# Kernel optimization log

Measured on AMD Instinct MI355X. Metric: run time of the kernel, lower is better.

## Reference

```python
import jax, jax.numpy as jnp
import numpy as np

N_MIX = 2


def setup_inputs() -> dict:
    key = jax.random.key(0)
    k1, k2, k3, k4 = jax.random.split(key, 4)
    B, d_k, N = 8, 512, 2048
    qt = jax.random.normal(k1, (B, d_k, N), dtype=jnp.float32)
    kt = jax.random.normal(k2, (B, d_k, N), dtype=jnp.float32)
    vt = jax.random.normal(k3, (B, d_k, N), dtype=jnp.float32)
    std = N_MIX ** -0.5
    weight = jax.random.uniform(k4, (N_MIX, d_k), dtype=jnp.float32, minval=-std, maxval=std)
    return {"qt": qt, "kt": kt, "vt": vt, "weight": weight}


def reference(qt, kt, vt, weight):
    # qt: [B, d_k, N], kt: [B, d_k, N2], vt: [B, d_v, N2], weight: [m, d_k]
    B, d_k, N = qt.shape
    N2 = kt.shape[2]
    m = N_MIX
    d = d_k // m
    temperature = jnp.float32(d_k ** 0.5)  # note: sqrt(d_k), not sqrt(d)

    # mixture weights pi: softmax over the m mixture components
    bar_qt = jnp.mean(qt, axis=2)  # [B, d_k]
    pi = jax.nn.softmax(jnp.einsum('md,bd->bm', weight, bar_qt), axis=1)  # [B, m]
    pi = pi.reshape(B * m, 1, 1)

    q = jnp.transpose(qt.reshape(B * m, d, N), (0, 2, 1))  # [B*m, N, d]
    k = kt.reshape(B * m, d, N2)                            # [B*m, d, N2]
    v = jnp.transpose(vt, (0, 2, 1))                        # [B, N2, d_v]

    attn = jnp.matmul(q, k) / temperature                   # [B*m, N, N2]
    attn = jax.nn.softmax(attn, axis=2)
    # dropout is identity at inference
    attn = (attn * pi).reshape(B, m, N, N2).sum(axis=1)     # [B, N, N2]

    output = jnp.matmul(attn, v)                            # [B, N, d_v]
    return output, attn
```

## Files before the change

kernel.cpp:

```cpp
#include <hip/hip_runtime.h>
#include <stdint.h>

typedef unsigned short u16;
typedef float f32x4 __attribute__((ext_vector_type(4)));
typedef _Float16 half8 __attribute__((ext_vector_type(8)));
typedef __fp16 fp16x2 __attribute__((ext_vector_type(2)));

#define B_  8
#define M_  2
#define DK_ 512
#define D_  256
#define N_  2048
#define DV_ 512

#define OUT_FLOATS (B_*N_*DV_)
#define QB_U16     (B_*M_*N_*D_)

__device__ __forceinline__ uint32_t pk16(float a, float b){
    fp16x2 h = __builtin_amdgcn_cvt_pkrtz(a, b);
    return __builtin_bit_cast(uint32_t, h);
}
__device__ __forceinline__ float h2f_lo(uint32_t u){
    return (float)__builtin_bit_cast(_Float16, (unsigned short)(u & 0xffffu));
}
__device__ __forceinline__ float h2f_hi(uint32_t u){
    return (float)__builtin_bit_cast(_Float16, (unsigned short)(u >> 16));
}

__global__ __launch_bounds__(256) void k0_transpose(const float* __restrict__ qt,
                                                    const float* __restrict__ kt,
                                                    u16* __restrict__ dstBase,
                                                    float* __restrict__ wsBar){
    const int it = blockIdx.x, yc = blockIdx.y, z = blockIdx.z;
    const int b = z & 7, src = z >> 3;
    const float* sp = src ? kt : qt;
    u16* dp = dstBase + (size_t)src * QB_U16;
    const int m = yc >> 2;
    const int cbase = (yc & 3) * 64;
    const int i0 = it * 64;
    __shared__ u16 lds[64 * 72];
    const int t = threadIdx.x;
    {
        const int c_loc = t >> 2;
        const int iq = (t & 3) * 16;
        const float* g = sp + (size_t)(b*DK_ + m*D_ + cbase + c_loc) * N_ + i0 + iq;
        float vv[16];
        *(float4*)&vv[0]  = *(const float4*)(g + 0);
        *(float4*)&vv[4]  = *(const float4*)(g + 4);
        *(float4*)&vv[8]  = *(const float4*)(g + 8);
        *(float4*)&vv[12] = *(const float4*)(g + 12);
        #pragma unroll
        for (int e = 0; e < 16; ++e){
            _Float16 hf = (_Float16)vv[e];
            lds[(iq + e)*72 + c_loc] = __builtin_bit_cast(unsigned short, hf);
        }
        if (src == 0){
            float s = 0.f;
            #pragma unroll
            for (int e = 0; e < 16; ++e) s += vv[e];
            s += __shfl_xor(s, 1);
            s += __shfl_xor(s, 2);
            if ((t & 3) == 0)
                atomicAdd(&wsBar[b*DK_ + m*D_ + cbase + c_loc], s);
        }
    }
    __syncthreads();
    {
        const int i_loc = t >> 2;
        const int cq = (t & 3) * 16;
        uint4 a  = *(const uint4*)&lds[i_loc*72 + cq];
        uint4 b2 = *(const uint4*)&lds[i_loc*72 + cq + 8];
        u16* o = dp + (size_t)((b*M_ + m)*N_ + i0 + i_loc) * D_ + cbase + cq;
        *(uint4*)o = a;
        *(uint4*)(o + 8) = b2;
    }
}

__global__ __launch_bounds__(256) void k0_vconv(const float* __restrict__ vt,
                                                u16* __restrict__ vF){
    const int idx = blockIdx.x * 256 + threadIdx.x;
    const int dv = idx & 511;
    const int g  = (idx >> 9) & 3;
    const int jc = (idx >> 11) & 63;
    const int b  = idx >> 17;
    const float* src = vt + ((size_t)(b*DV_ + dv))*N_ + jc*32 + g*8;
    float4 f0 = *(const float4*)src;
    float4 f1 = *(const float4*)(src + 4);
    uint4 o;
    o.x = pk16(f0.x, f0.y);
    o.y = pk16(f0.z, f0.w);
    o.z = pk16(f1.x, f1.y);
    o.w = pk16(f1.z, f1.w);
    *(uint4*)(vF + (size_t)idx * 8) = o;
}

__global__ void k2_logits(const float* __restrict__ wgt,
                          const float* __restrict__ bar,
                          float* __restrict__ wsLog){
    const int bm = blockIdx.x;
    const int b = bm >> 1, m = bm & 1;
    const int l = threadIdx.x;
    float s = 0.f;
    #pragma unroll
    for (int k = 0; k < 8; ++k){
        const int c = l + k*64;
        s += wgt[m*DK_ + c] * bar[b*DK_ + c];
    }
    s += __shfl_xor(s, 1); s += __shfl_xor(s, 2); s += __shfl_xor(s, 4);
    s += __shfl_xor(s, 8); s += __shfl_xor(s, 16); s += __shfl_xor(s, 32);
    if (l == 0) wsLog[bm] = s * (1.f / (float)N_);
}

__global__ __launch_bounds__(256, 2) void k3_qk(const u16* __restrict__ qB,
                                                const u16* __restrict__ kB,
                                                uint32_t* __restrict__ attnE,
                                                float* __restrict__ wsSum){
    const int jt = blockIdx.x, it = blockIdx.y, b = blockIdx.z;
    const int t = threadIdx.x;
    const int w = t >> 6, l = t & 63;
    const int wi = w & 1, wj = w >> 1;
    const int l15 = l & 15, lq = l >> 4;
    __shared__ u16 lds[4 * 128 * 64];

    f32x4 acc[2][4][4] = {};

    const int srow = t >> 1, shalf = t & 1;
    for (int bk = 0; bk < 4; ++bk){
        #pragma unroll
        for (int tile = 0; tile < 4; ++tile){
            const int qk = tile >> 1, m = tile & 1;
            const u16* sp = qk ? kB : qB;
            const int row0 = (qk ? jt : it) * 128;
            const u16* g = sp + (size_t)((b*M_ + m)*N_ + row0 + srow) * D_ + bk*64 + shalf*32;
            const uint4* gp = (const uint4*)g;
            uint4 v0 = gp[0], v1 = gp[1], v2 = gp[2], v3 = gp[3];
            u16* base = &lds[(tile*128 + srow) * 64];
            const int rs = srow & 7;
            *(uint4*)&base[((shalf*4 + 0) ^ rs) * 8] = v0;
            *(uint4*)&base[((shalf*4 + 1) ^ rs) * 8] = v1;
            *(uint4*)&base[((shalf*4 + 2) ^ rs) * 8] = v2;
            *(uint4*)&base[((shalf*4 + 3) ^ rs) * 8] = v3;
        }
        __syncthreads();
        #pragma unroll
        for (int ks = 0; ks < 2; ++ks){
            #pragma unroll
            for (int m = 0; m < 2; ++m){
                half8 a[4], bb[4];
                #pragma unroll
                for (int ti = 0; ti < 4; ++ti){
                    const int row = wi*64 + ti*16 + l15;
                    const int gr = (ks*4 + lq) ^ (row & 7);
                    a[ti] = *(const half8*)&lds[(m*128 + row)*64 + gr*8];
                }
                #pragma unroll
                for (int tj = 0; tj < 4; ++tj){
                    const int row = wj*64 + tj*16 + l15;
                    const int gr = (ks*4 + lq) ^ (row & 7);
                    bb[tj] = *(const half8*)&lds[((2 + m)*128 + row)*64 + gr*8];
                }
                #pragma unroll
                for (int ti = 0; ti < 4; ++ti)
                    #pragma unroll
                    for (int tj = 0; tj < 4; ++tj)
                        acc[m][ti][tj] = __builtin_amdgcn_mfma_f32_16x16x32_f16(
                            a[ti], bb[tj], acc[m][ti][tj], 0, 0, 0);
            }
        }
        __syncthreads();
    }

    const float INVT = 0.04419417382415922f;
    uint32_t* op = attnE + (size_t)b * N_ * N_;
    const int ibase = it*128 + wi*64;
    const int jbase = jt*128 + wj*64;
    #pragma unroll
    for (int ti = 0; ti < 4; ++ti){
        float rs[2][4] = {};
        #pragma unroll
        for (int tj = 0; tj < 4; ++tj){
            #pragma unroll
            for (int rr = 0; rr < 4; ++rr){
                const int i = ibase + ti*16 + lq*4 + rr;
                const int j = jbase + tj*16 + l15;
                const float e0 = __expf(acc[0][ti][tj][rr] * INVT);
                const float e1 = __expf(acc[1][ti][tj][rr] * INVT);
                op[(size_t)i * N_ + j] = pk16(e0, e1);
                rs[0][rr] += e0;
                rs[1][rr] += e1;
            }
        }
        #pragma unroll
        for (int m2 = 0; m2 < 2; ++m2){
            #pragma unroll
            for (int rr = 0; rr < 4; ++rr){
                float s = rs[m2][rr];
                s += __shfl_xor(s, 1); s += __shfl_xor(s, 2);
                s += __shfl_xor(s, 4); s += __shfl_xor(s, 8);
                if (l15 == 0)
                    atomicAdd(&wsSum[(size_t)(b*M_ + m2)*N_ + ibase + ti*16 + lq*4 + rr], s);
            }
        }
    }
}

template<bool HASVB>
__global__ __launch_bounds__(512) void k4_pv(const float* __restrict__ vt,
                                             const u16* __restrict__ vF,
                                             const float* __restrict__ wsLog,
                                             const float* __restrict__ wsSum,
                                             uint32_t* __restrict__ attnE,
                                             float* __restrict__ outO){
    const int tile = blockIdx.x, b = blockIdx.y;
    const int i0 = tile * 64;
    const int t = threadIdx.x, l = t & 63, w = t >> 6;
    const int l15 = l & 15, lq = l >> 4;
    const int rg = w >> 2, dvq = w & 3;
    __shared__ u16      vbuf[2][16384];
    __shared__ uint32_t ebuf[2][2048];
    __shared__ float    abuf[2][2048];

    const float lg0 = wsLog[b*2 + 0], lg1 = wsLog[b*2 + 1];
    const float pi0 = 1.f / (1.f + __expf(lg1 - lg0));
    const float pi1 = 1.f / (1.f + __expf(lg0 - lg1));

    float p0[2], p1[2];
    #pragma unroll
    for (int rh = 0; rh < 2; ++rh){
        const int row = i0 + rg*32 + rh*16 + l15;
        p0[rh] = pi0 / wsSum[(size_t)(b*M_ + 0)*N_ + row];
        p1[rh] = pi1 / wsSum[(size_t)(b*M_ + 1)*N_ + row];
    }

    const int crow = t >> 3, cg = t & 7, cgs = cg ^ (crow & 7);
    const uint32_t* egl = attnE + (size_t)(b*N_ + i0 + crow)*N_ + cg*4;
    float*          agl = (float*)attnE + (size_t)(b*N_ + i0 + crow)*N_ + cg*4;

    const u16*   vFb  = vF + (size_t)b * 64 * 16384;
    const float* vt32 = vt + (size_t)(b*DV_ + t)*N_;

    uint4  sv[4];
    float4 rf[8];
    uint4  er;

    auto loadV = [&](int c){
        if (HASVB){
            const u16* p = vFb + (size_t)c * 16384;
            #pragma unroll
            for (int k = 0; k < 4; ++k)
                sv[k] = *(const uint4*)(p + k*4096 + t*8);
        } else {
            const float4* p = (const float4*)(vt32 + c*32);
            #pragma unroll
            for (int q = 0; q < 8; ++q) rf[q] = p[q];
        }
    };
    auto writeV = [&](int buf){
        if (HASVB){
            #pragma unroll
            for (int k = 0; k < 4; ++k)
                *(uint4*)&vbuf[buf][k*4096 + t*8] = sv[k];
        } else {
            #pragma unroll
            for (int g = 0; g < 4; ++g){
                uint4 u;
                u.x = pk16(rf[2*g].x,   rf[2*g].y);
                u.y = pk16(rf[2*g].z,   rf[2*g].w);
                u.z = pk16(rf[2*g+1].x, rf[2*g+1].y);
                u.w = pk16(rf[2*g+1].z, rf[2*g+1].w);
                *(uint4*)&vbuf[buf][g*4096 + t*8] = u;
            }
        }
    };
    auto loadE  = [&](int c){ er = *(const uint4*)(egl + c*32); };
    auto writeE = [&](int buf){ *(uint4*)&ebuf[buf][crow*32 + cgs*4] = er; };

    f32x4 acc[2][8] = {};

    loadV(0); loadE(0);
    writeV(0); writeE(0);
    loadV(1); loadE(1);
    __syncthreads();

    for (int c = 0; c < 64; ++c){
        const int cur = c & 1;
        uint4 ef0[2], ef1[2];
        int gsa[2], gsb[2], rr_[2];
        #pragma unroll
        for (int rh = 0; rh < 2; ++rh){
            const int r = rg*32 + rh*16 + l15;
            gsa[rh] = (lq*2)     ^ (r & 7);
            gsb[rh] = (lq*2 + 1) ^ (r & 7);
            rr_[rh] = r;
            ef0[rh] = *(const uint4*)&ebuf[cur][r*32 + gsa[rh]*4];
            ef1[rh] = *(const uint4*)&ebuf[cur][r*32 + gsb[rh]*4];
        }
        if (c + 1 < 64){ writeV(cur ^ 1); writeE(cur ^ 1); }
        if (c + 2 < 64){ loadV(c + 2); loadE(c + 2); }

        float av[2][8];
        half8 af[2];
        #pragma unroll
        for (int rh = 0; rh < 2; ++rh){
            const uint4 u0 = ef0[rh], u1 = ef1[rh];
            av[rh][0] = p0[rh]*h2f_lo(u0.x) + p1[rh]*h2f_hi(u0.x);
            av[rh][1] = p0[rh]*h2f_lo(u0.y) + p1[rh]*h2f_hi(u0.y);
            av[rh][2] = p0[rh]*h2f_lo(u0.z) + p1[rh]*h2f_hi(u0.z);
            av[rh][3] = p0[rh]*h2f_lo(u0.w) + p1[rh]*h2f_hi(u0.w);
            av[rh][4] = p0[rh]*h2f_lo(u1.x) + p1[rh]*h2f_hi(u1.x);
            av[rh][5] = p0[rh]*h2f_lo(u1.y) + p1[rh]*h2f_hi(u1.y);
            av[rh][6] = p0[rh]*h2f_lo(u1.z) + p1[rh]*h2f_hi(u1.z);
            av[rh][7] = p0[rh]*h2f_lo(u1.w) + p1[rh]*h2f_hi(u1.w);
            uint4 ua;
            ua.x = pk16(av[rh][0], av[rh][1]);
            ua.y = pk16(av[rh][2], av[rh][3]);
            ua.z = pk16(av[rh][4], av[rh][5]);
            ua.w = pk16(av[rh][6], av[rh][7]);
            union { uint4 u; half8 h; } cv; cv.u = ua;
            af[rh] = cv.h;
        }
        if (dvq == 0){
            #pragma unroll
            for (int rh = 0; rh < 2; ++rh){
                *(float4*)&abuf[cur][rr_[rh]*32 + gsa[rh]*4] =
                    make_float4(av[rh][0], av[rh][1], av[rh][2], av[rh][3]);
                *(float4*)&abuf[cur][rr_[rh]*32 + gsb[rh]*4] =
                    make_float4(av[rh][4], av[rh][5], av[rh][6], av[rh][7]);
            }
        }
        if (c >= 1){
            float4 a = *(const float4*)&abuf[cur ^ 1][crow*32 + cgs*4];
            *(float4*)(agl + (c - 1)*32) = a;
        }
        const u16* vb = &vbuf[cur][lq*4096 + dvq*1024 + l15*8];
        #pragma unroll
        for (int n = 0; n < 8; ++n){
            half8 bv = *(const half8*)(vb + n*128);
            acc[0][n] = __builtin_amdgcn_mfma_f32_16x16x32_f16(af[0], bv, acc[0][n], 0, 0, 0);
            acc[1][n] = __builtin_amdgcn_mfma_f32_16x16x32_f16(af[1], bv, acc[1][n], 0, 0, 0);
        }
        __syncthreads();
    }
    {
        float4 a = *(const float4*)&abuf[1][crow*32 + cgs*4];
        *(float4*)(agl + 63*32) = a;
    }

    #pragma unroll
    for (int n = 0; n < 8; ++n){
        #pragma unroll
        for (int rh = 0; rh < 2; ++rh){
            #pragma unroll
            for (int rr = 0; rr < 4; ++rr){
                const int i  = i0 + rg*32 + rh*16 + lq*4 + rr;
                const int dv = dvq*128 + n*16 + l15;
                outO[(size_t)(b*N_ + i)*DV_ + dv] = acc[rh][n][rr];
            }
        }
    }
}

extern "C" void kernel_launch(void* const* d_in, const int* in_sizes, int n_in,
                              void* d_out, int out_size, void* d_ws, size_t ws_size,
                              hipStream_t stream){
    const float* qt  = (const float*)d_in[0];
    const float* kt  = (const float*)d_in[1];
    const float* vt  = (const float*)d_in[2];
    const float* wgt = (const float*)d_in[3];

    float* wsLog = (float*)d_ws;
    float* wsBar = (float*)((char*)d_ws + 4096);
    float* wsSum = (float*)((char*)d_ws + 65536);

    u16* stage = (u16*)d_out;
    u16* kB = stage + QB_U16;
    uint32_t* attnE = (uint32_t*)d_out + OUT_FLOATS;
    float* outO = (float*)d_out;

    const size_t vfBytes = (size_t)B_ * 64 * 16384 * 2;
    u16* vF = (ws_size >= (size_t)1048576 + vfBytes)
                  ? (u16*)((char*)d_ws + 1048576) : (u16*)nullptr;

    hipMemsetAsync(d_ws, 0, 262144, stream);

    k0_transpose<<<dim3(32, 8, 16), 256, 0, stream>>>(qt, kt, stage, wsBar);
    if (vF) k0_vconv<<<dim3(4096), 256, 0, stream>>>(vt, vF);
    k2_logits<<<dim3(16), 64, 0, stream>>>(wgt, wsBar, wsLog);
    k3_qk<<<dim3(16, 16, 8), 256, 0, stream>>>(stage, kB, attnE, wsSum);
    if (vF) k4_pv<true ><<<dim3(32, 8), 512, 0, stream>>>(vt, vF, wsLog, wsSum, attnE, outO);
    else    k4_pv<false><<<dim3(32, 8), 512, 0, stream>>>(vt, vF, wsLog, wsSum, attnE, outO);
}
```

Baseline: 250.9 us.

## Restructure PV kernel into 32-row tiles with direct register E loads

```diff
diff --git a/kernel.cpp b/kernel.cpp
--- a/kernel.cpp
+++ b/kernel.cpp
@@ -205,104 +205,93 @@
 }
 
 template<bool HASVB>
-__global__ __launch_bounds__(512) void k4_pv(const float* __restrict__ vt,
-                                             const u16* __restrict__ vF,
-                                             const float* __restrict__ wsLog,
-                                             const float* __restrict__ wsSum,
-                                             uint32_t* __restrict__ attnE,
-                                             float* __restrict__ outO){
-    const int tile = blockIdx.x, b = blockIdx.y;
-    const int i0 = tile * 64;
-    const int t = threadIdx.x, l = t & 63, w = t >> 6;
+__global__ __launch_bounds__(256, 2) void k4_pv(const float* __restrict__ vt,
+                                                const u16* __restrict__ vF,
+                                                const float* __restrict__ wsLog,
+                                                const float* __restrict__ wsSum,
+                                                uint32_t* __restrict__ attnE,
+                                                float* __restrict__ outO){
+    const int id = blockIdx.x;
+    const int b = id & 7, tile = id >> 3;
+    const int i0 = tile * 32;
+    const int t = threadIdx.x, l = t & 63, dvq = t >> 6;
     const int l15 = l & 15, lq = l >> 4;
-    const int rg = w >> 2, dvq = w & 3;
-    __shared__ u16      vbuf[2][16384];
-    __shared__ uint32_t ebuf[2][2048];
-    __shared__ float    abuf[2][2048];
+    __shared__ u16 vbuf[2][16384];
 
     const float lg0 = wsLog[b*2 + 0], lg1 = wsLog[b*2 + 1];
     const float pi0 = 1.f / (1.f + __expf(lg1 - lg0));
     const float pi1 = 1.f / (1.f + __expf(lg0 - lg1));
 
     float p0[2], p1[2];
+    uint32_t* erow[2];
     #pragma unroll
     for (int rh = 0; rh < 2; ++rh){
-        const int row = i0 + rg*32 + rh*16 + l15;
+        const int row = i0 + rh*16 + l15;
         p0[rh] = pi0 / wsSum[(size_t)(b*M_ + 0)*N_ + row];
         p1[rh] = pi1 / wsSum[(size_t)(b*M_ + 1)*N_ + row];
-    }
-
-    const int crow = t >> 3, cg = t & 7, cgs = cg ^ (crow & 7);
-    const uint32_t* egl = attnE + (size_t)(b*N_ + i0 + crow)*N_ + cg*4;
-    float*          agl = (float*)attnE + (size_t)(b*N_ + i0 + crow)*N_ + cg*4;
-
-    const u16*   vFb  = vF + (size_t)b * 64 * 16384;
-    const float* vt32 = vt + (size_t)(b*DV_ + t)*N_;
-
-    uint4  sv[4];
-    float4 rf[8];
-    uint4  er;
-
-    auto loadV = [&](int c){
+        erow[rh] = attnE + (size_t)(b*N_ + row) * N_;
+    }
+
+    const u16* vFb = vF + (size_t)b * (64 * 16384);
+
+    uint4 svA[8], svB[8], eA[4], eB[4];
+
+    auto loadV = [&](uint4 (&sv)[8], int c){
+        const u16* p = vFb + (size_t)c * 16384;
+        #pragma unroll
+        for (int q = 0; q < 8; ++q)
+            sv[q] = *(const uint4*)(p + q*2048 + t*8);
+    };
+    auto writeV = [&](int buf, uint4 (&sv)[8], int c){
         if (HASVB){
-            const u16* p = vFb + (size_t)c * 16384;
-            #pragma unroll
-            for (int k = 0; k < 4; ++k)
-                sv[k] = *(const uint4*)(p + k*4096 + t*8);
+            #pragma unroll
+            for (int q = 0; q < 8; ++q)
+                *(uint4*)&vbuf[buf][q*2048 + t*8] = sv[q];
         } else {
-            const float4* p = (const float4*)(vt32 + c*32);
-            #pragma unroll
-            for (int q = 0; q < 8; ++q) rf[q] = p[q];
+            const int d0 = t * 2;
+            #pragma unroll
+            for (int r = 0; r < 2; ++r){
+                const int dv = d0 + r;
+                const float* src = vt + (size_t)(b*DV_ + dv)*N_ + c*32;
+                #pragma unroll
+                for (int g = 0; g < 4; ++g){
+                    float4 f0 = *(const float4*)(src + g*8);
+                    float4 f1 = *(const float4*)(src + g*8 + 4);
+                    uint4 u;
+                    u.x = pk16(f0.x, f0.y); u.y = pk16(f0.z, f0.w);
+                    u.z = pk16(f1.x, f1.y); u.w = pk16(f1.z, f1.w);
+                    *(uint4*)&vbuf[buf][g*4096 + dv*8] = u;
+                }
+            }
         }
     };
-    auto writeV = [&](int buf){
-        if (HASVB){
-            #pragma unroll
-            for (int k = 0; k < 4; ++k)
-                *(uint4*)&vbuf[buf][k*4096 + t*8] = sv[k];
-        } else {
-            #pragma unroll
-            for (int g = 0; g < 4; ++g){
-                uint4 u;
-                u.x = pk16(rf[2*g].x,   rf[2*g].y);
-                u.y = pk16(rf[2*g].z,   rf[2*g].w);
-                u.z = pk16(rf[2*g+1].x, rf[2*g+1].y);
-                u.w = pk16(rf[2*g+1].z, rf[2*g+1].w);
-                *(uint4*)&vbuf[buf][g*4096 + t*8] = u;
-            }
+    auto loadE = [&](uint4 (&e)[4], int c){
+        #pragma unroll
+        for (int rh = 0; rh < 2; ++rh){
+            const uint4* p = (const uint4*)(erow[rh] + c*32 + lq*8);
+            e[rh*2 + 0] = p[0];
+            e[rh*2 + 1] = p[1];
         }
     };
-    auto loadE  = [&](int c){ er = *(const uint4*)(egl + c*32); };
-    auto writeE = [&](int buf){ *(uint4*)&ebuf[buf][crow*32 + cgs*4] = er; };
 
     f32x4 acc[2][8] = {};
 
-    loadV(0); loadE(0);
-    writeV(0); writeE(0);
-    loadV(1); loadE(1);
+    if (HASVB) loadV(svA, 0);
+    writeV(0, svA, 0);
+    if (HASVB) loadV(svB, 1);
+    loadE(eA, 0);
     __syncthreads();
 
-    for (int c = 0; c < 64; ++c){
-        const int cur = c & 1;
-        uint4 ef0[2], ef1[2];
-        int gsa[2], gsb[2], rr_[2];
-        #pragma unroll
-        for (int rh = 0; rh < 2; ++rh){
-            const int r = rg*32 + rh*16 + l15;
-            gsa[rh] = (lq*2)     ^ (r & 7);
-            gsb[rh] = (lq*2 + 1) ^ (r & 7);
-            rr_[rh] = r;
-            ef0[rh] = *(const uint4*)&ebuf[cur][r*32 + gsa[rh]*4];
-            ef1[rh] = *(const uint4*)&ebuf[cur][r*32 + gsb[rh]*4];
-        }
-        if (c + 1 < 64){ writeV(cur ^ 1); writeE(cur ^ 1); }
-        if (c + 2 < 64){ loadV(c + 2); loadE(c + 2); }
+    auto body = [&](int c, uint4 (&svW)[8], uint4 (&svL)[8],
+                    uint4 (&ec)[4], uint4 (&en)[4]){
+        if (HASVB && c + 2 < 64) loadV(svL, c + 2);
+        if (c + 1 < 64) loadE(en, c + 1);
 
         float av[2][8];
         half8 af[2];
         #pragma unroll
         for (int rh = 0; rh < 2; ++rh){
-            const uint4 u0 = ef0[rh], u1 = ef1[rh];
+            const uint4 u0 = ec[rh*2], u1 = ec[rh*2 + 1];
             av[rh][0] = p0[rh]*h2f_lo(u0.x) + p1[rh]*h2f_hi(u0.x);
             av[rh][1] = p0[rh]*h2f_lo(u0.y) + p1[rh]*h2f_hi(u0.y);
             av[rh][2] = p0[rh]*h2f_lo(u0.z) + p1[rh]*h2f_hi(u0.z);
@@ -319,31 +308,25 @@
             union { uint4 u; half8 h; } cv; cv.u = ua;
             af[rh] = cv.h;
         }
-        if (dvq == 0){
-            #pragma unroll
-            for (int rh = 0; rh < 2; ++rh){
-                *(float4*)&abuf[cur][rr_[rh]*32 + gsa[rh]*4] =
-                    make_float4(av[rh][0], av[rh][1], av[rh][2], av[rh][3]);
-                *(float4*)&abuf[cur][rr_[rh]*32 + gsb[rh]*4] =
-                    make_float4(av[rh][4], av[rh][5], av[rh][6], av[rh][7]);
-            }
-        }
-        if (c >= 1){
-            float4 a = *(const float4*)&abuf[cur ^ 1][crow*32 + cgs*4];
-            *(float4*)(agl + (c - 1)*32) = a;
-        }
-        const u16* vb = &vbuf[cur][lq*4096 + dvq*1024 + l15*8];
+        if (dvq < 2){
+            float* ap = (float*)(erow[dvq] + c*32 + lq*8);
+            *(float4*)ap       = make_float4(av[dvq][0], av[dvq][1], av[dvq][2], av[dvq][3]);
+            *(float4*)(ap + 4) = make_float4(av[dvq][4], av[dvq][5], av[dvq][6], av[dvq][7]);
+        }
+        const u16* vb = &vbuf[c & 1][lq*4096 + (dvq*128 + l15)*8];
         #pragma unroll
         for (int n = 0; n < 8; ++n){
             half8 bv = *(const half8*)(vb + n*128);
             acc[0][n] = __builtin_amdgcn_mfma_f32_16x16x32_f16(af[0], bv, acc[0][n], 0, 0, 0);
             acc[1][n] = __builtin_amdgcn_mfma_f32_16x16x32_f16(af[1], bv, acc[1][n], 0, 0, 0);
         }
+        if (c + 1 < 64) writeV((c + 1) & 1, svW, c + 1);
         __syncthreads();
-    }
-    {
-        float4 a = *(const float4*)&abuf[1][crow*32 + cgs*4];
-        *(float4*)(agl + 63*32) = a;
+    };
+
+    for (int c = 0; c < 64; c += 2){
+        body(c,     svB, svA, eA, eB);
+        body(c + 1, svA, svB, eB, eA);
     }
 
     #pragma unroll
@@ -352,7 +335,7 @@
         for (int rh = 0; rh < 2; ++rh){
             #pragma unroll
             for (int rr = 0; rr < 4; ++rr){
-                const int i  = i0 + rg*32 + rh*16 + lq*4 + rr;
+                const int i  = i0 + rh*16 + lq*4 + rr;
                 const int dv = dvq*128 + n*16 + l15;
                 outO[(size_t)(b*N_ + i)*DV_ + dv] = acc[rh][n][rr];
             }
@@ -387,6 +370,6 @@
     if (vF) k0_vconv<<<dim3(4096), 256, 0, stream>>>(vt, vF);
     k2_logits<<<dim3(16), 64, 0, stream>>>(wgt, wsBar, wsLog);
     k3_qk<<<dim3(16, 16, 8), 256, 0, stream>>>(stage, kB, attnE, wsSum);
-    if (vF) k4_pv<true ><<<dim3(32, 8), 512, 0, stream>>>(vt, vF, wsLog, wsSum, attnE, outO);
-    else    k4_pv<false><<<dim3(32, 8), 512, 0, stream>>>(vt, vF, wsLog, wsSum, attnE, outO);
-}
+    if (vF) k4_pv<true ><<<dim3(512), 256, 0, stream>>>(vt, vF, wsLog, wsSum, attnE, outO);
+    else    k4_pv<false><<<dim3(512), 256, 0, stream>>>(vt, vF, wsLog, wsSum, attnE, outO);
+}
```

Result: slower. 572.2 us (+128.0%).
